# Optimization experiments

Hardware: AMD Instinct MI355X
Metric: run time of the kernel (lower is better)

## Reference

```python
import jax, jax.numpy as jnp
import numpy as np

N_NODES = 1_000_000
N_EDGES = 16_000_000
NUM_REL = 3
C_IN, C_OUT = 3, 2


def setup_inputs() -> dict:
    key = jax.random.key(0)
    ks = jax.random.split(key, 10)
    x = jax.random.normal(ks[0], (N_NODES, C_IN), dtype=jnp.float32)
    edge_index = jax.random.randint(ks[1], (2, N_EDGES), 0, N_NODES, dtype=jnp.int64)
    edge_attr = jax.random.randint(ks[2], (N_EDGES,), 0, NUM_REL, dtype=jnp.int64)
    s = 0.3
    W1 = jax.random.normal(ks[3], (NUM_REL, C_IN, C_OUT), dtype=jnp.float32) * s
    root1 = jax.random.normal(ks[4], (C_IN, C_OUT), dtype=jnp.float32) * s
    b1 = jax.random.normal(ks[5], (C_OUT,), dtype=jnp.float32) * s
    W2 = jax.random.normal(ks[6], (NUM_REL, C_OUT, C_OUT), dtype=jnp.float32) * s
    root2 = jax.random.normal(ks[7], (C_OUT, C_OUT), dtype=jnp.float32) * s
    b2 = jax.random.normal(ks[8], (C_OUT,), dtype=jnp.float32) * s
    return {"x": x, "edge_index": edge_index, "edge_attr": edge_attr,
            "W1": W1, "root1": root1, "b1": b1,
            "W2": W2, "root2": root2, "b2": b2}


def rgcn_conv(x, edge_index, edge_type, W, root, bias, num_nodes):
    """PyG RGCNConv: per-relation mean-aggregated messages + root transform + bias."""
    src, dst = edge_index[0], edge_index[1]
    xs = x[src]                                    # [E, c_in] gather once
    out = x @ root + bias                          # [N, c_out]
    for r in range(NUM_REL):                       # small fixed relation loop
        mask = (edge_type == r)
        msg = jnp.where(mask[:, None], xs @ W[r], 0.0)          # [E, c_out]
        sums = jax.ops.segment_sum(msg, dst, num_segments=num_nodes)
        cnt = jax.ops.segment_sum(mask.astype(x.dtype), dst, num_segments=num_nodes)
        out = out + sums / jnp.maximum(cnt, 1.0)[:, None]       # mean aggr
    return out


def reference(x, edge_index, edge_attr, W1, root1, b1, W2, root2, b2):
    h = rgcn_conv(x, edge_index, edge_attr, W1, root1, b1, N_NODES)
    h = jax.nn.relu(h)
    # F.dropout(training=self.training): identity in eval mode
    out = rgcn_conv(h, edge_index, edge_attr, W2, root2, b2, N_NODES)
    return out
```

## Files before the change

kernel.cpp:

```cpp
#include <hip/hip_runtime.h>


typedef unsigned long long u64;
typedef unsigned u32;

constexpr int NN = 1000000;
constexpr int NE = 16000000;
constexpr int NR = 3;

constexpr int BSH   = 10;
constexpr int NB    = (NN + 1023) >> 10;
constexpr int BCAP  = 18432;
constexpr int EPB   = 16384;
constexpr int NBLKB = (NE + EPB - 1) / EPB;

__device__ __forceinline__ u32 enc_x(float x0, float x1, float x2) {
    int q0 = __float2int_rn(fminf(fmaxf(x0 * 64.0f, -511.0f), 511.0f));
    int q1 = __float2int_rn(fminf(fmaxf(x1 * 128.0f, -1023.0f), 1023.0f));
    int q2 = __float2int_rn(fminf(fmaxf(x2 * 128.0f, -1023.0f), 1023.0f));
    return ((u32)(q0 + 512) & 0x3FFu)
         | (((u32)(q1 + 1024) & 0x7FFu) << 10)
         | (((u32)(q2 + 1024) & 0x7FFu) << 21);
}

__device__ __forceinline__ u64 widen_x(u32 q) {
    return (u64)(q & 0x3FFu)
         | ((u64)((q >> 10) & 0x7FFu) << 18)
         | ((u64)(q >> 21) << 36)
         | (1ULL << 54);
}

__device__ __forceinline__ u32 enc_h(float h0, float h1) {
    int q0 = __float2int_rn(fminf(h0 * 1024.0f, 32767.0f));
    int q1 = __float2int_rn(fminf(h1 * 1024.0f, 32767.0f));
    return ((u32)q0 & 0xFFFFu) | ((u32)q1 << 16);
}

__device__ __forceinline__ u64 widen_h(u32 q) {
    return (u64)(q & 0xFFFFu)
         | ((u64)(q >> 16) << 22)
         | (1ULL << 44);
}

__device__ __forceinline__ void dec_h(u32 e, float& h0, float& h1) {
    h0 = (float)(e & 0xFFFFu) * (1.0f / 1024.0f);
    h1 = (float)(e >> 16)     * (1.0f / 1024.0f);
}

constexpr u64 M28 = (1ULL << 28) - 1;
__device__ __forceinline__ u64 pack_msg(float m0, float m1) {
    int a0 = __float2int_rn(fmaf(m0, 4096.0f, 524288.0f));
    int a1 = __float2int_rn(fmaf(m1, 4096.0f, 524288.0f));
    return (u64)(u32)a0 | ((u64)(u32)a1 << 28) | (1ULL << 56);
}


__global__ __launch_bounds__(1024) void scatter_kernel(
    const int* __restrict__ src, const int* __restrict__ dst, const int* __restrict__ rel,
    const float* __restrict__ x, u32* __restrict__ qx,
    u32* __restrict__ buf, u32* __restrict__ cursor)
{
    __shared__ u32 stage[EPB];
    __shared__ u32 hist[1024];
    __shared__ u32 wcur[1024];
    __shared__ u32 gbase[1024];
    __shared__ u32 wt[16];
    const int tid = threadIdx.x;
    const int wave = tid >> 6, lane = tid & 63;

    {
        int node = blockIdx.x * 1024 + tid;
        if (node < NN)
            qx[node] = enc_x(x[3 * node + 0], x[3 * node + 1], x[3 * node + 2]);
    }

    hist[tid] = 0;
    __syncthreads();

    const int base = blockIdx.x * EPB;
    const int nloc = min(EPB, NE - base);
    const int g4 = nloc >> 2;
    const int4* dp = (const int4*)(dst + base);
    const int4* sp = (const int4*)(src + base);
    const int4* rp = (const int4*)(rel + base);

    for (int i = tid; i < g4; i += 2048) {
        int4 a = dp[i];
        int j = i + 1024;
        if (j < g4) {
            int4 b = dp[j];
            atomicAdd(&hist[((u32)a.x) >> BSH], 1u);
            atomicAdd(&hist[((u32)a.y) >> BSH], 1u);
            atomicAdd(&hist[((u32)a.z) >> BSH], 1u);
            atomicAdd(&hist[((u32)a.w) >> BSH], 1u);
            atomicAdd(&hist[((u32)b.x) >> BSH], 1u);
            atomicAdd(&hist[((u32)b.y) >> BSH], 1u);
            atomicAdd(&hist[((u32)b.z) >> BSH], 1u);
            atomicAdd(&hist[((u32)b.w) >> BSH], 1u);
        } else {
            atomicAdd(&hist[((u32)a.x) >> BSH], 1u);
            atomicAdd(&hist[((u32)a.y) >> BSH], 1u);
            atomicAdd(&hist[((u32)a.z) >> BSH], 1u);
            atomicAdd(&hist[((u32)a.w) >> BSH], 1u);
        }
    }
    __syncthreads();

    {
        int h0 = hist[tid];
        int v0 = h0;
#pragma unroll
        for (int d = 1; d < 64; d <<= 1) {
            int t = __shfl_up(v0, d);
            if (lane >= d) v0 += t;
        }
        if (lane == 63) wt[wave] = (u32)v0;
        __syncthreads();
        u32 off = 0;
#pragma unroll
        for (int wv = 0; wv < 16; ++wv) off += (wv < wave) ? wt[wv] : 0u;
        wcur[tid] = off + (u32)(v0 - h0);
    }
    __syncthreads();

    if (tid < NB) {
        u32 c = hist[tid];
        gbase[tid] = c ? atomicAdd(&cursor[tid], c) : 0u;
    }
    __syncthreads();

    for (int i = tid; i < g4; i += 1024) {
        int4 d = dp[i];
        int4 s = sp[i];
        int4 r = rp[i];
        {
            u32 dd = (u32)d.x, bk = dd >> BSH;
            u32 sl = atomicAdd(&wcur[bk], 1u);
            stage[sl] = (u32)s.x | ((u32)r.x << 20) | ((dd & 1023u) << 22);
        }
        {
            u32 dd = (u32)d.y, bk = dd >> BSH;
            u32 sl = atomicAdd(&wcur[bk], 1u);
            stage[sl] = (u32)s.y | ((u32)r.y << 20) | ((dd & 1023u) << 22);
        }
        {
            u32 dd = (u32)d.z, bk = dd >> BSH;
            u32 sl = atomicAdd(&wcur[bk], 1u);
            stage[sl] = (u32)s.z | ((u32)r.z << 20) | ((dd & 1023u) << 22);
        }
        {
            u32 dd = (u32)d.w, bk = dd >> BSH;
            u32 sl = atomicAdd(&wcur[bk], 1u);
            stage[sl] = (u32)s.w | ((u32)r.w << 20) | ((dd & 1023u) << 22);
        }
    }
    __syncthreads();

    for (int b = wave; b < NB; b += 16) {
        u32 cnt = hist[b];
        if (!cnt) continue;
        u32 ls = wcur[b] - cnt;
        u32 gb = gbase[b];
        u32* bb = buf + (size_t)b * BCAP;
        for (u32 j = lane; j < cnt; j += 64) {
            u32 slot = gb + j;
            if (slot < (u32)BCAP) bb[slot] = stage[ls + j];
        }
    }
}

__global__ __launch_bounds__(512) void agg1_kernel(
    const u32* __restrict__ buf, const u32* __restrict__ cursor,
    const u32* __restrict__ qx, const float* __restrict__ x,
    const float* __restrict__ W1,
    const float* __restrict__ root1, const float* __restrict__ b1,
    u32* __restrict__ qh)
{
    __shared__ u64 acc[1024 * NR];
    __shared__ float w[NR * 3 * 2];
    const int tid = threadIdx.x;
    for (int i = tid; i < 1024 * NR; i += 512) acc[i] = 0;
    if (tid < NR * 3 * 2) w[tid] = W1[tid];
    __syncthreads();

    const int bk = blockIdx.x;
    const int n = min((int)cursor[bk], BCAP);
    const u32* bb = buf + (size_t)bk * BCAP;
    const int n8 = n >> 3;

    for (int g = tid; g < n8; g += 512) {
        const uint4* p = (const uint4*)(bb + ((size_t)g << 3));
        uint4 E0 = p[0], E1 = p[1];
        u32 e[8] = {E0.x, E0.y, E0.z, E0.w, E1.x, E1.y, E1.z, E1.w};
        u32 q[8];
#pragma unroll
        for (int j = 0; j < 8; ++j) q[j] = qx[e[j] & 0xFFFFFu];
#pragma unroll
        for (int j = 0; j < 8; ++j)
            atomicAdd(&acc[(e[j] >> 22) * NR + ((e[j] >> 20) & 3u)], widen_x(q[j]));
    }
    for (int i = (n8 << 3) + tid; i < n; i += 512) {
        u32 e0 = bb[i];
        u32 q0 = qx[e0 & 0xFFFFFu];
        atomicAdd(&acc[(e0 >> 22) * NR + ((e0 >> 20) & 3u)], widen_x(q0));
    }
    __syncthreads();

    for (int l = tid; l < 1024; l += 512) {
        int node = (bk << BSH) + l;
        if (node >= NN) continue;
        float x0 = x[3 * node + 0], x1 = x[3 * node + 1], x2 = x[3 * node + 2];
        float o0 = x0 * root1[0] + x1 * root1[2] + x2 * root1[4] + b1[0];
        float o1 = x0 * root1[1] + x1 * root1[3] + x2 * root1[5] + b1[1];
#pragma unroll
        for (int r = 0; r < NR; ++r) {
            u64 wv = acc[l * NR + r];
            u32 c = (u32)(wv >> 54);
            if (c) {
                float inv = 1.0f / (float)c;
                float S0 = (float)(u32)(wv & 0x3FFFFu);
                float S1 = (float)(u32)((wv >> 18) & 0x3FFFFu);
                float S2 = (float)(u32)((wv >> 36) & 0x3FFFFu);
                float m0 = fmaf(S0, inv, -512.0f)  * (1.0f / 64.0f);
                float m1 = fmaf(S1, inv, -1024.0f) * (1.0f / 128.0f);
                float m2 = fmaf(S2, inv, -1024.0f) * (1.0f / 128.0f);
                const float* wr = &w[r * 6];
                o0 += m0 * wr[0] + m1 * wr[2] + m2 * wr[4];
                o1 += m0 * wr[1] + m1 * wr[3] + m2 * wr[5];
            }
        }
        qh[node] = enc_h(fmaxf(o0, 0.0f), fmaxf(o1, 0.0f));
    }
}

__global__ __launch_bounds__(512) void agg2_kernel(
    const u32* __restrict__ buf, const u32* __restrict__ cursor,
    const u32* __restrict__ qh, const float* __restrict__ W2,
    const float* __restrict__ root2, const float* __restrict__ b2,
    float* __restrict__ out)
{
    __shared__ u64 acc[1024 * NR];
    __shared__ float w[NR * 2 * 2];
    const int tid = threadIdx.x;
    for (int i = tid; i < 1024 * NR; i += 512) acc[i] = 0;
    if (tid < NR * 2 * 2) w[tid] = W2[tid];
    __syncthreads();

    const int bk = blockIdx.x;
    const int n = min((int)cursor[bk], BCAP);
    const u32* bb = buf + (size_t)bk * BCAP;
    const int n8 = n >> 3;

    for (int g = tid; g < n8; g += 512) {
        const uint4* p = (const uint4*)(bb + ((size_t)g << 3));
        uint4 E0 = p[0], E1 = p[1];
        u32 e[8] = {E0.x, E0.y, E0.z, E0.w, E1.x, E1.y, E1.z, E1.w};
        u32 q[8];
#pragma unroll
        for (int j = 0; j < 8; ++j) q[j] = qh[e[j] & 0xFFFFFu];
#pragma unroll
        for (int j = 0; j < 8; ++j)
            atomicAdd(&acc[(e[j] >> 22) * NR + ((e[j] >> 20) & 3u)], widen_h(q[j]));
    }
    for (int i = (n8 << 3) + tid; i < n; i += 512) {
        u32 e0 = bb[i];
        u32 q0 = qh[e0 & 0xFFFFFu];
        atomicAdd(&acc[(e0 >> 22) * NR + ((e0 >> 20) & 3u)], widen_h(q0));
    }
    __syncthreads();

    for (int l = tid; l < 1024; l += 512) {
        int node = (bk << BSH) + l;
        if (node >= NN) continue;
        float hv0, hv1;
        dec_h(qh[node], hv0, hv1);
        float o0 = hv0 * root2[0] + hv1 * root2[2] + b2[0];
        float o1 = hv0 * root2[1] + hv1 * root2[3] + b2[1];
#pragma unroll
        for (int r = 0; r < NR; ++r) {
            u64 wv = acc[l * NR + r];
            u32 c = (u32)(wv >> 44);
            if (c) {
                float inv = 1.0f / (float)c;
                float m0 = (float)(u32)(wv & 0x3FFFFFu)         * inv * (1.0f / 1024.0f);
                float m1 = (float)(u32)((wv >> 22) & 0x3FFFFFu) * inv * (1.0f / 1024.0f);
                const float* wr = &w[r * 4];
                o0 += m0 * wr[0] + m1 * wr[2];
                o1 += m0 * wr[1] + m1 * wr[3];
            }
        }
        float2 ov; ov.x = o0; ov.y = o1;
        ((float2*)out)[node] = ov;
    }
}


__global__ __launch_bounds__(256) void edge1_kernel(
    const int* __restrict__ src, const int* __restrict__ dst, const int* __restrict__ rel,
    const float* __restrict__ x, const float* __restrict__ W1,
    u64* __restrict__ sums1)
{
    __shared__ float w[NR * 3 * 2];
    if (threadIdx.x < NR * 3 * 2) w[threadIdx.x] = W1[threadIdx.x];
    __syncthreads();
    int e = blockIdx.x * 256 + threadIdx.x;
    if (e >= NE) return;
    int s = src[e], d = dst[e], r = rel[e];
    float x0 = x[3 * s + 0], x1 = x[3 * s + 1], x2 = x[3 * s + 2];
    const float* wr = &w[r * 6];
    float m0 = x0 * wr[0] + x1 * wr[2] + x2 * wr[4];
    float m1 = x0 * wr[1] + x1 * wr[3] + x2 * wr[5];
    atomicAdd(&sums1[d * NR + r], pack_msg(m0, m1));
}

__global__ __launch_bounds__(256) void node1_kernel(
    const float* __restrict__ x, const u64* __restrict__ sums1,
    const float* __restrict__ root1, const float* __restrict__ b1,
    float* __restrict__ h)
{
    int n = blockIdx.x * 256 + threadIdx.x;
    if (n >= NN) return;
    float x0 = x[3 * n + 0], x1 = x[3 * n + 1], x2 = x[3 * n + 2];
    float o0 = x0 * root1[0] + x1 * root1[2] + x2 * root1[4] + b1[0];
    float o1 = x0 * root1[1] + x1 * root1[3] + x2 * root1[5] + b1[1];
#pragma unroll
    for (int r = 0; r < NR; ++r) {
        u64 wv = sums1[n * NR + r];
        int c = (int)(wv >> 56);
        int s0i = (int)(wv & M28) - (c << 19);
        int s1i = (int)((wv >> 28) & M28) - (c << 19);
        float inv = (1.0f / 4096.0f) / (float)(c > 1 ? c : 1);
        o0 += (float)s0i * inv;
        o1 += (float)s1i * inv;
    }
    float2 hv;
    hv.x = fmaxf(o0, 0.0f);
    hv.y = fmaxf(o1, 0.0f);
    ((float2*)h)[n] = hv;
}

__global__ __launch_bounds__(256) void edge2_kernel(
    const int* __restrict__ src, const int* __restrict__ dst, const int* __restrict__ rel,
    const float* __restrict__ h, const float* __restrict__ W2,
    u64* __restrict__ sums2)
{
    __shared__ float w[NR * 2 * 2];
    if (threadIdx.x < NR * 2 * 2) w[threadIdx.x] = W2[threadIdx.x];
    __syncthreads();
    int e = blockIdx.x * 256 + threadIdx.x;
    if (e >= NE) return;
    int s = src[e];
    float2 hs = ((const float2*)h)[s];
    if (hs.x == 0.0f && hs.y == 0.0f) return;
    int d = dst[e], r = rel[e];
    const float* wr = &w[r * 4];
    float m0 = hs.x * wr[0] + hs.y * wr[2];
    float m1 = hs.x * wr[1] + hs.y * wr[3];
    atomicAdd(&sums2[d * NR + r], pack_msg(m0, m1));
}

__global__ __launch_bounds__(256) void node2_kernel(
    const float* __restrict__ h, const u64* __restrict__ sums1, const u64* __restrict__ sums2,
    const float* __restrict__ root2, const float* __restrict__ b2,
    float* __restrict__ out)
{
    int n = blockIdx.x * 256 + threadIdx.x;
    if (n >= NN) return;
    float2 hv = ((const float2*)h)[n];
    float o0 = hv.x * root2[0] + hv.y * root2[2] + b2[0];
    float o1 = hv.x * root2[1] + hv.y * root2[3] + b2[1];
#pragma unroll
    for (int r = 0; r < NR; ++r) {
        u64 w1 = sums1[n * NR + r];
        u64 w2 = sums2[n * NR + r];
        int c    = (int)(w1 >> 56);
        int adds = (int)(w2 >> 56);
        int s0i = (int)(w2 & M28) - (adds << 19);
        int s1i = (int)((w2 >> 28) & M28) - (adds << 19);
        float inv = (1.0f / 4096.0f) / (float)(c > 1 ? c : 1);
        o0 += (float)s0i * inv;
        o1 += (float)s1i * inv;
    }
    float2 ov; ov.x = o0; ov.y = o1;
    ((float2*)out)[n] = ov;
}

extern "C" void kernel_launch(void* const* d_in, const int* in_sizes, int n_in,
                              void* d_out, int out_size, void* d_ws, size_t ws_size,
                              hipStream_t stream) {
    const float* x     = (const float*)d_in[0];
    const int*   ei    = (const int*)d_in[1];
    const int*   rel   = (const int*)d_in[2];
    const float* W1    = (const float*)d_in[3];
    const float* root1 = (const float*)d_in[4];
    const float* b1    = (const float*)d_in[5];
    const float* W2    = (const float*)d_in[6];
    const float* root2 = (const float*)d_in[7];
    const float* b2    = (const float*)d_in[8];
    float* out = (float*)d_out;

    const int* src = ei;
    const int* dst = ei + NE;

    char* ws = (char*)d_ws;
    const int nb = (NN + 255) / 256;

    const size_t OFF_QX  = 72024064;
    const size_t OFF_QH  = 76024064;
    const size_t OFF_CUR = 80024064;
    const size_t WS_NEED = OFF_CUR + (size_t)NB * sizeof(u32);

    if (ws_size >= WS_NEED) {
        u32* buf    = (u32*)ws;
        u32* qx     = (u32*)(ws + OFF_QX);
        u32* qh     = (u32*)(ws + OFF_QH);
        u32* cursor = (u32*)(ws + OFF_CUR);

        hipMemsetAsync(cursor, 0, (size_t)NB * sizeof(u32), stream);
        scatter_kernel<<<NBLKB, 1024, 0, stream>>>(src, dst, rel, x, qx, buf, cursor);
        agg1_kernel<<<NB, 512, 0, stream>>>(buf, cursor, qx, x, W1, root1, b1, qh);
        agg2_kernel<<<NB, 512, 0, stream>>>(buf, cursor, qh, W2, root2, b2, out);
    } else {
        u64*   sums1 = (u64*)ws;
        u64*   sums2 = (u64*)(ws + (size_t)24 * 1000 * 1000);
        float* h     = (float*)(ws + (size_t)48 * 1000 * 1000);
        const int eb = (NE + 255) / 256;

        hipMemsetAsync(sums1, 0, (size_t)NN * NR * sizeof(u64), stream);
        hipMemsetAsync(sums2, 0, (size_t)NN * NR * sizeof(u64), stream);
        edge1_kernel<<<eb, 256, 0, stream>>>(src, dst, rel, x, W1, sums1);
        node1_kernel<<<nb, 256, 0, stream>>>(x, sums1, root1, b1, h);
        edge2_kernel<<<eb, 256, 0, stream>>>(src, dst, rel, h, W2, sums2);
        node2_kernel<<<nb, 256, 0, stream>>>(h, sums1, sums2, root2, b2, out);
    }
}
```

Measured before the change: 464.4 us.

## Fuse scatter and two aggregation passes into one cooperative persistent kernel

Replaces the three-kernel pipeline (bucket scatter, layer-1 aggregation, layer-2 aggregation) with a single cooperative kernel. It loops persistently over tiles and separates the phases with grid-wide syncs, reusing one shared memory region for the staging buffers and the accumulators. The aim is to remove kernel launch gaps and tail effects between phases. The cost is that the grid is capped at occupancy, about 256 CUs times the blocks allowed per CU, which may reduce parallelism in the aggregation phases, and grid.sync itself adds overhead.

```diff
diff --git a/kernel.cpp b/kernel.cpp
--- a/kernel.cpp
+++ b/kernel.cpp
@@ -1,4 +1,7 @@
 #include <hip/hip_runtime.h>
+#include <hip/hip_cooperative_groups.h>
+
+namespace cg = cooperative_groups;
 
 
 typedef unsigned long long u64;
@@ -52,6 +55,252 @@
     int a0 = __float2int_rn(fmaf(m0, 4096.0f, 524288.0f));
     int a1 = __float2int_rn(fmaf(m1, 4096.0f, 524288.0f));
     return (u64)(u32)a0 | ((u64)(u32)a1 << 28) | (1ULL << 56);
+}
+
+
+constexpr int SMEM_U64 = 9736;
+
+__global__ __launch_bounds__(1024, 8) void fused_kernel(
+    const int* __restrict__ src, const int* __restrict__ dst, const int* __restrict__ rel,
+    const float* __restrict__ x, u32* __restrict__ qx,
+    u32* __restrict__ buf, u32* __restrict__ cursor,
+    const float* __restrict__ W1, const float* __restrict__ root1, const float* __restrict__ b1,
+    u32* __restrict__ qh,
+    const float* __restrict__ W2, const float* __restrict__ root2, const float* __restrict__ b2,
+    float* __restrict__ out)
+{
+    __shared__ u64 smem[SMEM_U64];
+    u32* stage = (u32*)smem;
+    u32* hist  = stage + EPB;
+    u32* wcur  = hist + 1024;
+    u32* gbase = wcur + 1024;
+    u32* wt    = gbase + 1024;
+    u64* acc   = smem;
+    float* wsh = (float*)(smem + 1024 * NR);
+
+    cg::grid_group grid = cg::this_grid();
+    const int tid  = threadIdx.x;
+    const int wave = tid >> 6, lane = tid & 63;
+    const int nblk = gridDim.x;
+
+    for (int t = blockIdx.x; t < NBLKB; t += nblk) {
+        {
+            int node = t * 1024 + tid;
+            if (node < NN)
+                qx[node] = enc_x(x[3 * node + 0], x[3 * node + 1], x[3 * node + 2]);
+        }
+
+        hist[tid] = 0;
+        __syncthreads();
+
+        const int base = t * EPB;
+        const int nloc = min(EPB, NE - base);
+        const int g4 = nloc >> 2;
+        const int4* dp = (const int4*)(dst + base);
+        const int4* sp = (const int4*)(src + base);
+        const int4* rp = (const int4*)(rel + base);
+
+        for (int i = tid; i < g4; i += 2048) {
+            int4 a = dp[i];
+            int j = i + 1024;
+            if (j < g4) {
+                int4 b = dp[j];
+                atomicAdd(&hist[((u32)a.x) >> BSH], 1u);
+                atomicAdd(&hist[((u32)a.y) >> BSH], 1u);
+                atomicAdd(&hist[((u32)a.z) >> BSH], 1u);
+                atomicAdd(&hist[((u32)a.w) >> BSH], 1u);
+                atomicAdd(&hist[((u32)b.x) >> BSH], 1u);
+                atomicAdd(&hist[((u32)b.y) >> BSH], 1u);
+                atomicAdd(&hist[((u32)b.z) >> BSH], 1u);
+                atomicAdd(&hist[((u32)b.w) >> BSH], 1u);
+            } else {
+                atomicAdd(&hist[((u32)a.x) >> BSH], 1u);
+                atomicAdd(&hist[((u32)a.y) >> BSH], 1u);
+                atomicAdd(&hist[((u32)a.z) >> BSH], 1u);
+                atomicAdd(&hist[((u32)a.w) >> BSH], 1u);
+            }
+        }
+        __syncthreads();
+
+        {
+            int h0 = hist[tid];
+            int v0 = h0;
+#pragma unroll
+            for (int d = 1; d < 64; d <<= 1) {
+                int tt = __shfl_up(v0, d);
+                if (lane >= d) v0 += tt;
+            }
+            if (lane == 63) wt[wave] = (u32)v0;
+            __syncthreads();
+            u32 off = 0;
+#pragma unroll
+            for (int wv = 0; wv < 16; ++wv) off += (wv < wave) ? wt[wv] : 0u;
+            wcur[tid] = off + (u32)(v0 - h0);
+        }
+        __syncthreads();
+
+        if (tid < NB) {
+            u32 c = hist[tid];
+            gbase[tid] = c ? atomicAdd(&cursor[tid], c) : 0u;
+        }
+        __syncthreads();
+
+        for (int i = tid; i < g4; i += 1024) {
+            int4 d = dp[i];
+            int4 s = sp[i];
+            int4 r = rp[i];
+            {
+                u32 dd = (u32)d.x, bk = dd >> BSH;
+                u32 sl = atomicAdd(&wcur[bk], 1u);
+                stage[sl] = (u32)s.x | ((u32)r.x << 20) | ((dd & 1023u) << 22);
+            }
+            {
+                u32 dd = (u32)d.y, bk = dd >> BSH;
+                u32 sl = atomicAdd(&wcur[bk], 1u);
+                stage[sl] = (u32)s.y | ((u32)r.y << 20) | ((dd & 1023u) << 22);
+            }
+            {
+                u32 dd = (u32)d.z, bk = dd >> BSH;
+                u32 sl = atomicAdd(&wcur[bk], 1u);
+                stage[sl] = (u32)s.z | ((u32)r.z << 20) | ((dd & 1023u) << 22);
+            }
+            {
+                u32 dd = (u32)d.w, bk = dd >> BSH;
+                u32 sl = atomicAdd(&wcur[bk], 1u);
+                stage[sl] = (u32)s.w | ((u32)r.w << 20) | ((dd & 1023u) << 22);
+            }
+        }
+        __syncthreads();
+
+        for (int b = wave; b < NB; b += 16) {
+            u32 cnt = hist[b];
+            if (!cnt) continue;
+            u32 ls = wcur[b] - cnt;
+            u32 gb = gbase[b];
+            u32* bb = buf + (size_t)b * BCAP;
+            for (u32 j = lane; j < cnt; j += 64) {
+                u32 slot = gb + j;
+                if (slot < (u32)BCAP) bb[slot] = stage[ls + j];
+            }
+        }
+        __syncthreads();
+    }
+
+    __threadfence();
+    grid.sync();
+
+    for (int bk = blockIdx.x; bk < NB; bk += nblk) {
+        for (int i = tid; i < 1024 * NR; i += 1024) acc[i] = 0;
+        if (tid < NR * 3 * 2) wsh[tid] = W1[tid];
+        __syncthreads();
+
+        const int n = min((int)cursor[bk], BCAP);
+        const u32* bb = buf + (size_t)bk * BCAP;
+        const int n8 = n >> 3;
+
+        for (int g = tid; g < n8; g += 1024) {
+            const uint4* p = (const uint4*)(bb + ((size_t)g << 3));
+            uint4 E0 = p[0], E1 = p[1];
+            u32 e[8] = {E0.x, E0.y, E0.z, E0.w, E1.x, E1.y, E1.z, E1.w};
+            u32 q[8];
+#pragma unroll
+            for (int j = 0; j < 8; ++j) q[j] = qx[e[j] & 0xFFFFFu];
+#pragma unroll
+            for (int j = 0; j < 8; ++j)
+                atomicAdd(&acc[(e[j] >> 22) * NR + ((e[j] >> 20) & 3u)], widen_x(q[j]));
+        }
+        for (int i = (n8 << 3) + tid; i < n; i += 1024) {
+            u32 e0 = bb[i];
+            u32 q0 = qx[e0 & 0xFFFFFu];
+            atomicAdd(&acc[(e0 >> 22) * NR + ((e0 >> 20) & 3u)], widen_x(q0));
+        }
+        __syncthreads();
+
+        {
+            int node = (bk << BSH) + tid;
+            if (node < NN) {
+                float x0 = x[3 * node + 0], x1 = x[3 * node + 1], x2 = x[3 * node + 2];
+                float o0 = x0 * root1[0] + x1 * root1[2] + x2 * root1[4] + b1[0];
+                float o1 = x0 * root1[1] + x1 * root1[3] + x2 * root1[5] + b1[1];
+#pragma unroll
+                for (int r = 0; r < NR; ++r) {
+                    u64 wv = acc[tid * NR + r];
+                    u32 c = (u32)(wv >> 54);
+                    if (c) {
+                        float inv = 1.0f / (float)c;
+                        float S0 = (float)(u32)(wv & 0x3FFFFu);
+                        float S1 = (float)(u32)((wv >> 18) & 0x3FFFFu);
+                        float S2 = (float)(u32)((wv >> 36) & 0x3FFFFu);
+                        float m0 = fmaf(S0, inv, -512.0f)  * (1.0f / 64.0f);
+                        float m1 = fmaf(S1, inv, -1024.0f) * (1.0f / 128.0f);
+                        float m2 = fmaf(S2, inv, -1024.0f) * (1.0f / 128.0f);
+                        const float* wr = &wsh[r * 6];
+                        o0 += m0 * wr[0] + m1 * wr[2] + m2 * wr[4];
+                        o1 += m0 * wr[1] + m1 * wr[3] + m2 * wr[5];
+                    }
+                }
+                qh[node] = enc_h(fmaxf(o0, 0.0f), fmaxf(o1, 0.0f));
+            }
+        }
+        __syncthreads();
+    }
+
+    __threadfence();
+    grid.sync();
+
+    for (int bk = blockIdx.x; bk < NB; bk += nblk) {
+        for (int i = tid; i < 1024 * NR; i += 1024) acc[i] = 0;
+        if (tid < NR * 2 * 2) wsh[tid] = W2[tid];
+        __syncthreads();
+
+        const int n = min((int)cursor[bk], BCAP);
+        const u32* bb = buf + (size_t)bk * BCAP;
+        const int n8 = n >> 3;
+
+        for (int g = tid; g < n8; g += 1024) {
+            const uint4* p = (const uint4*)(bb + ((size_t)g << 3));
+            uint4 E0 = p[0], E1 = p[1];
+            u32 e[8] = {E0.x, E0.y, E0.z, E0.w, E1.x, E1.y, E1.z, E1.w};
+            u32 q[8];
+#pragma unroll
+            for (int j = 0; j < 8; ++j) q[j] = qh[e[j] & 0xFFFFFu];
+#pragma unroll
+            for (int j = 0; j < 8; ++j)
+                atomicAdd(&acc[(e[j] >> 22) * NR + ((e[j] >> 20) & 3u)], widen_h(q[j]));
+        }
+        for (int i = (n8 << 3) + tid; i < n; i += 1024) {
+            u32 e0 = bb[i];
+            u32 q0 = qh[e0 & 0xFFFFFu];
+            atomicAdd(&acc[(e0 >> 22) * NR + ((e0 >> 20) & 3u)], widen_h(q0));
+        }
+        __syncthreads();
+
+        {
+            int node = (bk << BSH) + tid;
+            if (node < NN) {
+                float hv0, hv1;
+                dec_h(qh[node], hv0, hv1);
+                float o0 = hv0 * root2[0] + hv1 * root2[2] + b2[0];
+                float o1 = hv0 * root2[1] + hv1 * root2[3] + b2[1];
+#pragma unroll
+                for (int r = 0; r < NR; ++r) {
+                    u64 wv = acc[tid * NR + r];
+                    u32 c = (u32)(wv >> 44);
+                    if (c) {
+                        float inv = 1.0f / (float)c;
+                        float m0 = (float)(u32)(wv & 0x3FFFFFu)         * inv * (1.0f / 1024.0f);
+                        float m1 = (float)(u32)((wv >> 22) & 0x3FFFFFu) * inv * (1.0f / 1024.0f);
+                        const float* wr = &wsh[r * 4];
+                        o0 += m0 * wr[0] + m1 * wr[2];
+                        o1 += m0 * wr[1] + m1 * wr[3];
+                    }
+                }
+                float2 ov; ov.x = o0; ov.y = o1;
+                ((float2*)out)[node] = ov;
+            }
+        }
+        __syncthreads();
+    }
 }
 
 
@@ -417,9 +666,28 @@
         u32* cursor = (u32*)(ws + OFF_CUR);
 
         hipMemsetAsync(cursor, 0, (size_t)NB * sizeof(u32), stream);
-        scatter_kernel<<<NBLKB, 1024, 0, stream>>>(src, dst, rel, x, qx, buf, cursor);
-        agg1_kernel<<<NB, 512, 0, stream>>>(buf, cursor, qx, x, W1, root1, b1, qh);
-        agg2_kernel<<<NB, 512, 0, stream>>>(buf, cursor, qh, W2, root2, b2, out);
+
+        bool done = false;
+        int maxb = 0;
+        hipError_t qe = hipOccupancyMaxActiveBlocksPerMultiprocessor(
+            &maxb, fused_kernel, 1024, 0);
+        if (qe == hipSuccess && maxb >= 1) {
+            int gridn = maxb * 256;
+            if (gridn > NBLKB) gridn = NBLKB;
+            void* kargs[] = {
+                (void*)&src, (void*)&dst, (void*)&rel, (void*)&x, (void*)&qx,
+                (void*)&buf, (void*)&cursor,
+                (void*)&W1, (void*)&root1, (void*)&b1, (void*)&qh,
+                (void*)&W2, (void*)&root2, (void*)&b2, (void*)&out };
+            hipError_t le = hipLaunchCooperativeKernel(
+                (void*)fused_kernel, dim3(gridn), dim3(1024), kargs, 0u, stream);
+            done = (le == hipSuccess);
+        }
+        if (!done) {
+            scatter_kernel<<<NBLKB, 1024, 0, stream>>>(src, dst, rel, x, qx, buf, cursor);
+            agg1_kernel<<<NB, 512, 0, stream>>>(buf, cursor, qx, x, W1, root1, b1, qh);
+            agg2_kernel<<<NB, 512, 0, stream>>>(buf, cursor, qh, W2, root2, b2, out);
+        }
     } else {
         u64*   sums1 = (u64*)ws;
         u64*   sums2 = (u64*)(ws + (size_t)24 * 1000 * 1000);
```

After: 743.9 us. +60.2%, slower.
